# Kernel optimization log

Hardware: AMD Instinct MI355X
Metric: run time of the kernel (lower is better)

The kernel has to match this reference:

```python
import jax, jax.numpy as jnp
import numpy as np

N = 100000   # nodes
E = 1600000  # message edges (avg degree 16)
L = 500000   # supervision (label) edges
IN = 128     # input feature dim
H = 2        # attention heads
C = 64       # hidden_dim per head
HC = H * C   # 128, per-layer output channels
DEC = 64     # decoder_dim
NEG_SLOPE = 0.2


def setup_inputs():
    key = jax.random.key(0)
    ks = jax.random.split(key, 16)
    s = 0.05
    return {
        "x": jax.random.normal(ks[0], (N, IN), jnp.float32),
        "edge_index": jax.random.randint(ks[1], (2, E), 0, N, dtype=jnp.int64),
        "edge_label_index": jax.random.randint(ks[2], (2, L), 0, N, dtype=jnp.int64),
        "W1": jax.random.normal(ks[3], (IN, HC), jnp.float32) * s,
        "att_src1": jax.random.normal(ks[4], (H, C), jnp.float32) * s,
        "att_dst1": jax.random.normal(ks[5], (H, C), jnp.float32) * s,
        "bias1": jnp.zeros((HC,), jnp.float32),
        "W2": jax.random.normal(ks[6], (HC, HC), jnp.float32) * s,
        "att_src2": jax.random.normal(ks[7], (H, C), jnp.float32) * s,
        "att_dst2": jax.random.normal(ks[8], (H, C), jnp.float32) * s,
        "bias2": jnp.zeros((HC,), jnp.float32),
        "lin1_w": jax.random.normal(ks[9], (2 * HC, DEC), jnp.float32) * s,
        "lin1_b": jnp.zeros((DEC,), jnp.float32),
        "lin2_w": jax.random.normal(ks[10], (DEC, 1), jnp.float32) * s,
        "lin2_b": jnp.zeros((1,), jnp.float32),
    }


def _gat_conv(x, src, dst, W, att_src, att_dst, bias, n_nodes):
    # PyG GATConv (concat=True, negative_slope=0.2), self-loops already in src/dst.
    h = (x @ W).reshape(-1, H, C)                       # [N, H, C]
    a_s = jnp.sum(h * att_src[None], axis=-1)           # [N, H]
    a_d = jnp.sum(h * att_dst[None], axis=-1)           # [N, H]
    e = jax.nn.leaky_relu(a_s[src] + a_d[dst], NEG_SLOPE)  # [E, H]
    m = jax.ops.segment_max(e, dst, num_segments=n_nodes)  # segment-softmax (stable)
    ex = jnp.exp(e - jax.lax.stop_gradient(m)[dst])
    denom = jax.ops.segment_sum(ex, dst, num_segments=n_nodes)
    alpha = ex / denom[dst]                             # [E, H]
    out = jax.ops.segment_sum(h[src] * alpha[:, :, None], dst, num_segments=n_nodes)
    return out.reshape(n_nodes, HC) + bias


def reference(x, edge_index, edge_label_index, W1, att_src1, att_dst1, bias1,
              W2, att_src2, att_dst2, bias2, lin1_w, lin1_b, lin2_w, lin2_b):
    n = x.shape[0]
    loop = jnp.arange(n, dtype=edge_index.dtype)
    src = jnp.concatenate([edge_index[0], loop])
    dst = jnp.concatenate([edge_index[1], loop])
    # encode (eval mode: dropout is a no-op)
    h1 = jax.nn.relu(_gat_conv(x, src, dst, W1, att_src1, att_dst1, bias1, n))
    z = _gat_conv(h1, src, dst, W2, att_src2, att_dst2, bias2, n)
    # decode
    hs = jnp.concatenate([z[edge_label_index[0]], z[edge_label_index[1]]], axis=1)
    hdec = jax.nn.relu(hs @ lin1_w + lin1_b)
    return (hdec @ lin2_w + lin2_b).reshape(-1)
```

## Files before the change

### kernel.cpp

```cpp
#include <hip/hip_runtime.h>
#include <hip/hip_fp16.h>


typedef _Float16 f16x8 __attribute__((ext_vector_type(8)));
typedef float f32x4 __attribute__((ext_vector_type(4)));

__device__ __forceinline__ float rl_f(float v, int lane) {
    return __int_as_float(__builtin_amdgcn_readlane(__float_as_int(v), lane));
}

__device__ __forceinline__ void fma_mix_lo(float& acc, unsigned hv, float e) {
    asm("v_fma_mix_f32 %0, %1, %2, %0 op_sel_hi:[1,0,0]"
        : "+v"(acc) : "v"(hv), "v"(e));
}
__device__ __forceinline__ void fma_mix_hi(float& acc, unsigned hv, float e) {
    asm("v_fma_mix_f32 %0, %1, %2, %0 op_sel:[1,0,0] op_sel_hi:[1,0,0]"
        : "+v"(acc) : "v"(hv), "v"(e));
}

#define WT_LD 136
__global__ __launch_bounds__(256, 3) void gemm_mfma(
    const float* __restrict__ X, const float* __restrict__ W,
    _Float16* __restrict__ Y, int nrows,
    const float* __restrict__ att_s, const float* __restrict__ att_d,
    float2* __restrict__ as_out, float2* __restrict__ ad_out)
{
    __shared__ _Float16 WT[128 * WT_LD];
    __shared__ _Float16 At[64 * WT_LD];
    const int t = threadIdx.x;
    const int lane = t & 63;
    const int wid = t >> 6;

    for (int i = t; i < 128 * 32; i += 256) {
        const int k = i >> 5;
        const int n4 = (i & 31) * 4;
        const float4 wv = *reinterpret_cast<const float4*>(&W[k * 128 + n4]);
        WT[(n4 + 0) * WT_LD + k] = (_Float16)wv.x;
        WT[(n4 + 1) * WT_LD + k] = (_Float16)wv.y;
        WT[(n4 + 2) * WT_LD + k] = (_Float16)wv.z;
        WT[(n4 + 3) * WT_LD + k] = (_Float16)wv.w;
    }

    const int am = lane & 15, ag = lane >> 4;

    float asv[8], adv[8];
    if (as_out) {
#pragma unroll
        for (int n0 = 0; n0 < 8; ++n0) {
            asv[n0] = att_s[n0 * 16 + am];
            adv[n0] = att_d[n0 * 16 + am];
        }
    }

    const int ntiles = (nrows + 63) >> 6;
    for (int tile = blockIdx.x; tile < ntiles; tile += gridDim.x) {
        const int rbase = tile * 64;
        __syncthreads();
        {
            const int r = t >> 2;
            const int c0 = (t & 3) * 32;
            const int gr = rbase + r;
            _Float16 tmp[32];
            if (gr < nrows) {
                const float* src = X + (size_t)gr * 128 + c0;
#pragma unroll
                for (int q = 0; q < 8; ++q) {
                    const float4 v = *reinterpret_cast<const float4*>(src + q * 4);
                    tmp[q * 4 + 0] = (_Float16)v.x; tmp[q * 4 + 1] = (_Float16)v.y;
                    tmp[q * 4 + 2] = (_Float16)v.z; tmp[q * 4 + 3] = (_Float16)v.w;
                }
            } else {
#pragma unroll
                for (int q = 0; q < 32; ++q) tmp[q] = (_Float16)0.f;
            }
#pragma unroll
            for (int q = 0; q < 4; ++q)
                *reinterpret_cast<f16x8*>(&At[r * WT_LD + c0 + q * 8]) =
                    *reinterpret_cast<const f16x8*>(&tmp[q * 8]);
        }
        __syncthreads();

        const int srow = wid * 16;
        f16x8 a[4];
#pragma unroll
        for (int kb = 0; kb < 4; ++kb)
            a[kb] = *reinterpret_cast<const f16x8*>(
                &At[(srow + am) * WT_LD + kb * 32 + ag * 8]);

        f32x4 acc[8];
#pragma unroll
        for (int n0 = 0; n0 < 8; ++n0) {
            f32x4 c = {0.f, 0.f, 0.f, 0.f};
#pragma unroll
            for (int kb = 0; kb < 4; ++kb) {
                const f16x8 b = *reinterpret_cast<const f16x8*>(
                    &WT[(n0 * 16 + am) * WT_LD + kb * 32 + ag * 8]);
                c = __builtin_amdgcn_mfma_f32_16x16x32_f16(a[kb], b, c, 0, 0, 0);
            }
            acc[n0] = c;
        }

        const int growbase = rbase + srow + ag * 4;

#pragma unroll
        for (int j = 0; j < 4; ++j) {
            const int grow = growbase + j;
            if (grow < nrows) {
#pragma unroll
                for (int n0 = 0; n0 < 8; ++n0)
                    Y[(size_t)grow * 128 + n0 * 16 + am] = (_Float16)acc[n0][j];
            }
        }

        if (as_out) {
#pragma unroll
            for (int j = 0; j < 4; ++j) {
                float s0 = 0.f, s1 = 0.f, d0 = 0.f, d1 = 0.f;
#pragma unroll
                for (int n0 = 0; n0 < 4; ++n0) {
                    s0 = fmaf(acc[n0][j], asv[n0], s0);
                    d0 = fmaf(acc[n0][j], adv[n0], d0);
                }
#pragma unroll
                for (int n0 = 4; n0 < 8; ++n0) {
                    s1 = fmaf(acc[n0][j], asv[n0], s1);
                    d1 = fmaf(acc[n0][j], adv[n0], d1);
                }
#pragma unroll
                for (int off = 1; off < 16; off <<= 1) {
                    s0 += __shfl_xor(s0, off, 64); s1 += __shfl_xor(s1, off, 64);
                    d0 += __shfl_xor(d0, off, 64); d1 += __shfl_xor(d1, off, 64);
                }
                const int grow = growbase + j;
                if (am == 0 && grow < nrows) {
                    as_out[grow] = make_float2(s0, s1);
                    ad_out[grow] = make_float2(d0, d1);
                }
            }
        }
    }
}

__global__ __launch_bounds__(256) void init_counts_k(int* __restrict__ counts, int N)
{
    const int i = blockIdx.x * blockDim.x + threadIdx.x;
    if (i < N) counts[i] = 1;
}

__global__ __launch_bounds__(256) void hist_xcd_k(
    const int* __restrict__ edst, int E, int* __restrict__ counts, int npp)
{
    const int part = blockIdx.x & 7;
    const int lo = part * npp;
    const int hiN = lo + npp;
    const int bi = blockIdx.x >> 3;
    const int stride = (gridDim.x >> 3) * blockDim.x;
    for (int e = bi * blockDim.x + threadIdx.x; e < E; e += stride) {
        const int d = edst[e];
        if (d >= lo && d < hiN) atomicAdd(&counts[d], 1);
    }
}

__global__ __launch_bounds__(256) void scan_phase1(
    const int* __restrict__ counts, int* __restrict__ blockSums, int N)
{
    __shared__ int wsum[4];
    const int b = blockIdx.x, t = threadIdx.x;
    const int base = b * 1024 + t * 4;
    int s = 0;
    if (base + 3 < N) {
        const int4 c = *reinterpret_cast<const int4*>(&counts[base]);
        s = c.x + c.y + c.z + c.w;
    } else {
#pragma unroll
        for (int k = 0; k < 4; ++k) if (base + k < N) s += counts[base + k];
    }
#pragma unroll
    for (int off = 32; off; off >>= 1) s += __shfl_xor(s, off, 64);
    if ((t & 63) == 0) wsum[t >> 6] = s;
    __syncthreads();
    if (t == 0) blockSums[b] = wsum[0] + wsum[1] + wsum[2] + wsum[3];
}

__global__ __launch_bounds__(256) void scan_phase2(
    int* __restrict__ blockSums, int nb, int* __restrict__ row_ptr, int N)
{
    __shared__ int wsum[4];
    __shared__ int carry_sh;
    const int t = threadIdx.x;
    if (t == 0) carry_sh = 0;
    __syncthreads();
    for (int base = 0; base < nb; base += 256) {
        const int i = base + t;
        const int v = (i < nb) ? blockSums[i] : 0;
        int x = v;
#pragma unroll
        for (int off = 1; off < 64; off <<= 1) {
            const int y = __shfl_up(x, off, 64);
            if ((t & 63) >= off) x += y;
        }
        if ((t & 63) == 63) wsum[t >> 6] = x;
        __syncthreads();
        int woff = 0;
        for (int w = 0; w < (t >> 6); ++w) woff += wsum[w];
        const int carry = carry_sh;
        if (i < nb) blockSums[i] = carry + woff + x - v;
        __syncthreads();
        if (t == 255) carry_sh = carry + woff + x;
        __syncthreads();
    }
    if (t == 0) row_ptr[N] = carry_sh;
}

__global__ __launch_bounds__(256) void scan_phase3(
    const int* __restrict__ counts, const int* __restrict__ blockSums,
    int* __restrict__ row_ptr, int N)
{
    __shared__ int wsum[4];
    const int b = blockIdx.x, t = threadIdx.x;
    const int base = b * 1024 + t * 4;
    int v0 = 0, v1 = 0, v2 = 0, v3 = 0;
    if (base + 3 < N) {
        const int4 c = *reinterpret_cast<const int4*>(&counts[base]);
        v0 = c.x; v1 = c.y; v2 = c.z; v3 = c.w;
    } else {
        if (base + 0 < N) v0 = counts[base + 0];
        if (base + 1 < N) v1 = counts[base + 1];
        if (base + 2 < N) v2 = counts[base + 2];
        if (base + 3 < N) v3 = counts[base + 3];
    }
    const int tsum = v0 + v1 + v2 + v3;
    int x = tsum;
#pragma unroll
    for (int off = 1; off < 64; off <<= 1) {
        const int y = __shfl_up(x, off, 64);
        if ((t & 63) >= off) x += y;
    }
    if ((t & 63) == 63) wsum[t >> 6] = x;
    __syncthreads();
    int woff = 0;
    for (int w = 0; w < (t >> 6); ++w) woff += wsum[w];
    int excl = blockSums[b] + woff + x - tsum;
    if (base + 0 < N) row_ptr[base + 0] = excl;
    if (base + 1 < N) row_ptr[base + 1] = excl + v0;
    if (base + 2 < N) row_ptr[base + 2] = excl + v0 + v1;
    if (base + 3 < N) row_ptr[base + 3] = excl + v0 + v1 + v2;
}

__global__ __launch_bounds__(256) void init_cursor_k(
    const int* __restrict__ row_ptr, int* __restrict__ cursor,
    int* __restrict__ csr_src, int N)
{
    const int i = blockIdx.x * blockDim.x + threadIdx.x;
    if (i < N) {
        const int p = row_ptr[i];
        csr_src[p] = i;
        cursor[i] = p + 1;
    }
}

__global__ __launch_bounds__(256) void scatter_xcd_k(
    const int* __restrict__ esrc, const int* __restrict__ edst, int E,
    int* __restrict__ cursor, int* __restrict__ csr_src, int npp)
{
    const int part = blockIdx.x & 7;
    const int lo = part * npp;
    const int hiN = lo + npp;
    const int bi = blockIdx.x >> 3;
    const int stride = (gridDim.x >> 3) * blockDim.x;
    for (int e = bi * blockDim.x + threadIdx.x; e < E; e += stride) {
        const int d = edst[e];
        if (d >= lo && d < hiN) {
            const int pos = atomicAdd(&cursor[d], 1);
            csr_src[pos] = esrc[e];
        }
    }
}

__global__ __launch_bounds__(256) void csr_aggregate(
    const int* __restrict__ row_ptr, const int* __restrict__ csr_src,
    const unsigned* __restrict__ h2u, const float2* __restrict__ as_,
    const float2* __restrict__ ad_, const float* __restrict__ bias,
    float* __restrict__ out, int N, int do_relu)
{
    const int lane = threadIdx.x & 63;
    const int node = (blockIdx.x * blockDim.x + threadIdx.x) >> 6;
    if (node >= N) return;
    const int l32 = lane & 31;
    const int half = lane >> 5;
    const bool head1 = l32 >= 16;

    const int start = row_ptr[node];
    const int end   = row_ptr[node + 1];
    const float2 ad = ad_[node];

    float den0 = 0.f, den1 = 0.f;
    float acc0 = 0.f, acc1 = 0.f, acc2 = 0.f, acc3 = 0.f;

    for (int base = start; base < end; base += 64) {
        const int cnt = min(64, end - base);
        float ex0 = 0.f, ex1 = 0.f;
        int s = 0;
        if (lane < cnt) {
            s = csr_src[base + lane];
            const float2 as = as_[s];
            float e0 = as.x + ad.x; e0 = fmaxf(e0, 0.2f * e0);
            float e1 = as.y + ad.y; e1 = fmaxf(e1, 0.2f * e1);
            ex0 = __expf(e0); ex1 = __expf(e1);
            den0 += ex0; den1 += ex1;
        }
        int j = 0;
        for (; j + 8 <= cnt; j += 8) {
            uint2 hv[4]; float e[4];
#pragma unroll
            for (int q = 0; q < 4; ++q) {
                const int jA = j + 2 * q, jB = jA + 1;
                const int sA = __builtin_amdgcn_readlane(s, jA);
                const int sB = __builtin_amdgcn_readlane(s, jB);
                const float eA = head1 ? rl_f(ex1, jA) : rl_f(ex0, jA);
                const float eB = head1 ? rl_f(ex1, jB) : rl_f(ex0, jB);
                e[q] = half ? eB : eA;
                const int src = half ? sB : sA;
                hv[q] = *reinterpret_cast<const uint2*>(
                    h2u + (unsigned)(src * 64 + l32 * 2));
            }
#pragma unroll
            for (int q = 0; q < 4; ++q) {
                fma_mix_lo(acc0, hv[q].x, e[q]);
                fma_mix_hi(acc1, hv[q].x, e[q]);
                fma_mix_lo(acc2, hv[q].y, e[q]);
                fma_mix_hi(acc3, hv[q].y, e[q]);
            }
        }
        for (; j < cnt; j += 2) {
            const int jA = j, jB = j + 1;
            const int sA = __builtin_amdgcn_readlane(s, jA);
            const int sB = __builtin_amdgcn_readlane(s, jB);
            const float eA = head1 ? rl_f(ex1, jA) : rl_f(ex0, jA);
            const float eB = head1 ? rl_f(ex1, jB) : rl_f(ex0, jB);
            const float e = half ? eB : eA;
            const int src = half ? sB : sA;
            const uint2 hv = *reinterpret_cast<const uint2*>(
                h2u + (unsigned)(src * 64 + l32 * 2));
            fma_mix_lo(acc0, hv.x, e);
            fma_mix_hi(acc1, hv.x, e);
            fma_mix_lo(acc2, hv.y, e);
            fma_mix_hi(acc3, hv.y, e);
        }
    }

    acc0 += __shfl_xor(acc0, 32, 64);
    acc1 += __shfl_xor(acc1, 32, 64);
    acc2 += __shfl_xor(acc2, 32, 64);
    acc3 += __shfl_xor(acc3, 32, 64);

#pragma unroll
    for (int off = 32; off; off >>= 1) {
        den0 += __shfl_xor(den0, off, 64);
        den1 += __shfl_xor(den1, off, 64);
    }

    if (half == 0) {
        const float rd = 1.f / (head1 ? den1 : den0);
        const float4 bv = *reinterpret_cast<const float4*>(&bias[l32 * 4]);
        float4 v;
        v.x = fmaf(acc0, rd, bv.x);
        v.y = fmaf(acc1, rd, bv.y);
        v.z = fmaf(acc2, rd, bv.z);
        v.w = fmaf(acc3, rd, bv.w);
        if (do_relu) {
            v.x = fmaxf(v.x, 0.f); v.y = fmaxf(v.y, 0.f);
            v.z = fmaxf(v.z, 0.f); v.w = fmaxf(v.w, 0.f);
        }
        *reinterpret_cast<float4*>(&out[(size_t)node * 128 + l32 * 4]) = v;
    }
}

__global__ void build_wuv(const float* __restrict__ lin1_w, float* __restrict__ Wuv)
{
    const int i = blockIdx.x * blockDim.x + threadIdx.x;
    if (i >= 128 * 128) return;
    const int k = i >> 7, j = i & 127;
    Wuv[i] = (j < 64) ? lin1_w[k * 64 + j] : lin1_w[(128 + k) * 64 + (j - 64)];
}

__global__ __launch_bounds__(256) void decode_k(
    const int* __restrict__ eli, int L_, const unsigned* __restrict__ uvd,
    const float* __restrict__ lin1_b, const float* __restrict__ lin2_w,
    const float* __restrict__ lin2_b, float* __restrict__ out)
{
    const int lane = threadIdx.x & 63;
    const int l32 = lane & 31;
    const int half = lane >> 5;
    const int pstride = (gridDim.x * blockDim.x) >> 6;
    const float2 bv = ((const float2*)lin1_b)[l32];
    const float2 wv = ((const float2*)lin2_w)[l32];
    const float b2 = lin2_b[0];
    const int npairs = (L_ + 1) >> 1;
    for (int pid = (blockIdx.x * blockDim.x + threadIdx.x) >> 6; pid < npairs; pid += pstride) {
        const int w = min(pid * 2 + half, L_ - 1);
        const int a = eli[w], b = eli[L_ + w];
        const unsigned ua = uvd[(unsigned)(a * 64 + l32)];
        const unsigned vb = uvd[(unsigned)(b * 64 + 32 + l32)];
        float x0 = bv.x, x1 = bv.y;
        asm("v_fma_mix_f32 %0, %1, 1.0, %0 op_sel_hi:[1,0,0]" : "+v"(x0) : "v"(ua));
        asm("v_fma_mix_f32 %0, %1, 1.0, %0 op_sel:[1,0,0] op_sel_hi:[1,0,0]" : "+v"(x1) : "v"(ua));
        asm("v_fma_mix_f32 %0, %1, 1.0, %0 op_sel_hi:[1,0,0]" : "+v"(x0) : "v"(vb));
        asm("v_fma_mix_f32 %0, %1, 1.0, %0 op_sel:[1,0,0] op_sel_hi:[1,0,0]" : "+v"(x1) : "v"(vb));
        x0 = fmaxf(x0, 0.f); x1 = fmaxf(x1, 0.f);
        float p = fmaf(x0, wv.x, x1 * wv.y);
#pragma unroll
        for (int off = 1; off < 32; off <<= 1) p += __shfl_xor(p, off, 64);
        if (l32 == 0 && pid * 2 + half < L_) out[pid * 2 + half] = p + b2;
    }
}

extern "C" void kernel_launch(void* const* d_in, const int* in_sizes, int n_in,
                              void* d_out, int out_size, void* d_ws, size_t ws_size,
                              hipStream_t stream)
{
    const float* x     = (const float*)d_in[0];
    const int*   ei    = (const int*)d_in[1];
    const int*   eli   = (const int*)d_in[2];
    const float* W1    = (const float*)d_in[3];
    const float* atts1 = (const float*)d_in[4];
    const float* attd1 = (const float*)d_in[5];
    const float* bias1 = (const float*)d_in[6];
    const float* W2    = (const float*)d_in[7];
    const float* atts2 = (const float*)d_in[8];
    const float* attd2 = (const float*)d_in[9];
    const float* bias2 = (const float*)d_in[10];
    const float* lin1w = (const float*)d_in[11];
    const float* lin1b = (const float*)d_in[12];
    const float* lin2w = (const float*)d_in[13];
    const float* lin2b = (const float*)d_in[14];
    float* out = (float*)d_out;

    const int N = in_sizes[0] / 128;
    const int E = in_sizes[1] / 2;
    const int L = in_sizes[2] / 2;

    float* ws   = (float*)d_ws;
    __half2* h16 = (__half2*)ws;
    float* x2z  = ws + (size_t)N * 64;
    float* a_s  = x2z + (size_t)N * 128;
    float* a_d  = a_s + (size_t)N * 2;
    float* Wuv  = a_d + (size_t)N * 2;
    int* row_ptr = (int*)(Wuv + 128 * 128);
    int* counts  = row_ptr + (N + 4);
    int* cursor  = counts + N;
    int* csr_src = cursor + N;
    int* blockSums = csr_src + (E + N);

    const int nBlocks256 = (N + 255) / 256;
    const int nb = (N + 1023) / 1024;
    const int npp = (N + 7) / 8;
    const int ntiles = (N + 63) / 64;
    const int gemmGrid = ntiles < 768 ? ntiles : 768;

    init_counts_k<<<nBlocks256, 256, 0, stream>>>(counts, N);
    hist_xcd_k<<<2048, 256, 0, stream>>>(ei + E, E, counts, npp);
    scan_phase1<<<nb, 256, 0, stream>>>(counts, blockSums, N);
    scan_phase2<<<1, 256, 0, stream>>>(blockSums, nb, row_ptr, N);
    scan_phase3<<<nb, 256, 0, stream>>>(counts, blockSums, row_ptr, N);
    init_cursor_k<<<nBlocks256, 256, 0, stream>>>(row_ptr, cursor, csr_src, N);
    scatter_xcd_k<<<2048, 256, 0, stream>>>(ei, ei + E, E, cursor, csr_src, npp);

    for (int layer = 0; layer < 2; ++layer) {
        const float* xin  = (layer == 0) ? x : x2z;
        const float* W    = (layer == 0) ? W1 : W2;
        const float* as_w = (layer == 0) ? atts1 : atts2;
        const float* ad_w = (layer == 0) ? attd1 : attd2;
        const float* bs   = (layer == 0) ? bias1 : bias2;

        gemm_mfma<<<gemmGrid, 256, 0, stream>>>(xin, W, (_Float16*)h16, N, as_w, ad_w,
                                                (float2*)a_s, (float2*)a_d);
        csr_aggregate<<<(N + 3) / 4, 256, 0, stream>>>(row_ptr, csr_src,
                                                       (const unsigned*)h16,
                                                       (const float2*)a_s, (const float2*)a_d,
                                                       bs, x2z, N, (layer == 0) ? 1 : 0);
    }

    build_wuv<<<64, 256, 0, stream>>>(lin1w, Wuv);
    gemm_mfma<<<gemmGrid, 256, 0, stream>>>(x2z, Wuv, (_Float16*)h16, N,
                                            nullptr, nullptr, nullptr, nullptr);
    decode_k<<<8192, 256, 0, stream>>>(eli, L, (const unsigned*)h16,
                                       lin1b, lin2w, lin2b, out);
}
```

Baseline: 438.0 us.

## Prefetch next GEMM tile into registers and fuse CSR init into scan

The GEMM kernel now loads the next 64-row tile of X into registers while the MFMA work on the current tile runs, hiding global-load latency in the persistent loop at the cost of extra registers. CSR construction drops the counts-init and cursor-init kernels. Counts are zeroed with a memset, the self-loop +1 is added inside the scan phases, and scan_phase3 writes row_ptr, the self-loop csr_src entry and the cursor directly. This removes two kernel launches and one pass over row_ptr.

Measured after the change: 431.0 us. About the same (-1.6%).

```diff
diff --git a/kernel.cpp b/kernel.cpp
--- a/kernel.cpp
+++ b/kernel.cpp
@@ -42,6 +42,8 @@
     }
 
     const int am = lane & 15, ag = lane >> 4;
+    const int pr = t >> 2;
+    const int pc = (t & 3) * 32;
 
     float asv[8], adv[8];
     if (as_out) {
@@ -52,33 +54,44 @@
         }
     }
 
+    float4 pf[8];
+    auto load_pf = [&](int tbase) {
+        const int gr = tbase + pr;
+        if (gr < nrows) {
+            const float* src = X + (size_t)gr * 128 + pc;
+#pragma unroll
+            for (int q = 0; q < 8; ++q)
+                pf[q] = *reinterpret_cast<const float4*>(src + q * 4);
+        } else {
+#pragma unroll
+            for (int q = 0; q < 8; ++q) pf[q] = make_float4(0.f, 0.f, 0.f, 0.f);
+        }
+    };
+    auto write_pf = [&]() {
+        _Float16 tmp[32];
+#pragma unroll
+        for (int q = 0; q < 8; ++q) {
+            tmp[q * 4 + 0] = (_Float16)pf[q].x; tmp[q * 4 + 1] = (_Float16)pf[q].y;
+            tmp[q * 4 + 2] = (_Float16)pf[q].z; tmp[q * 4 + 3] = (_Float16)pf[q].w;
+        }
+#pragma unroll
+        for (int q = 0; q < 4; ++q)
+            *reinterpret_cast<f16x8*>(&At[pr * WT_LD + pc + q * 8]) =
+                *reinterpret_cast<const f16x8*>(&tmp[q * 8]);
+    };
+
     const int ntiles = (nrows + 63) >> 6;
-    for (int tile = blockIdx.x; tile < ntiles; tile += gridDim.x) {
+    int tile = blockIdx.x;
+    if (tile < ntiles) load_pf(tile * 64);
+
+    for (; tile < ntiles; tile += gridDim.x) {
         const int rbase = tile * 64;
         __syncthreads();
-        {
-            const int r = t >> 2;
-            const int c0 = (t & 3) * 32;
-            const int gr = rbase + r;
-            _Float16 tmp[32];
-            if (gr < nrows) {
-                const float* src = X + (size_t)gr * 128 + c0;
-#pragma unroll
-                for (int q = 0; q < 8; ++q) {
-                    const float4 v = *reinterpret_cast<const float4*>(src + q * 4);
-                    tmp[q * 4 + 0] = (_Float16)v.x; tmp[q * 4 + 1] = (_Float16)v.y;
-                    tmp[q * 4 + 2] = (_Float16)v.z; tmp[q * 4 + 3] = (_Float16)v.w;
-                }
-            } else {
-#pragma unroll
-                for (int q = 0; q < 32; ++q) tmp[q] = (_Float16)0.f;
-            }
-#pragma unroll
-            for (int q = 0; q < 4; ++q)
-                *reinterpret_cast<f16x8*>(&At[r * WT_LD + c0 + q * 8]) =
-                    *reinterpret_cast<const f16x8*>(&tmp[q * 8]);
-        }
+        write_pf();
         __syncthreads();
+
+        const int nt = tile + gridDim.x;
+        if (nt < ntiles) load_pf(nt * 64);
 
         const int srow = wid * 16;
         f16x8 a[4];
@@ -141,12 +154,6 @@
     }
 }
 
-__global__ __launch_bounds__(256) void init_counts_k(int* __restrict__ counts, int N)
-{
-    const int i = blockIdx.x * blockDim.x + threadIdx.x;
-    if (i < N) counts[i] = 1;
-}
-
 __global__ __launch_bounds__(256) void hist_xcd_k(
     const int* __restrict__ edst, int E, int* __restrict__ counts, int npp)
 {
@@ -170,10 +177,10 @@
     int s = 0;
     if (base + 3 < N) {
         const int4 c = *reinterpret_cast<const int4*>(&counts[base]);
-        s = c.x + c.y + c.z + c.w;
+        s = c.x + c.y + c.z + c.w + 4;
     } else {
 #pragma unroll
-        for (int k = 0; k < 4; ++k) if (base + k < N) s += counts[base + k];
+        for (int k = 0; k < 4; ++k) if (base + k < N) s += counts[base + k] + 1;
     }
 #pragma unroll
     for (int off = 32; off; off >>= 1) s += __shfl_xor(s, off, 64);
@@ -214,7 +221,8 @@
 
 __global__ __launch_bounds__(256) void scan_phase3(
     const int* __restrict__ counts, const int* __restrict__ blockSums,
-    int* __restrict__ row_ptr, int N)
+    int* __restrict__ row_ptr, int* __restrict__ cursor,
+    int* __restrict__ csr_src, int N)
 {
     __shared__ int wsum[4];
     const int b = blockIdx.x, t = threadIdx.x;
@@ -222,12 +230,12 @@
     int v0 = 0, v1 = 0, v2 = 0, v3 = 0;
     if (base + 3 < N) {
         const int4 c = *reinterpret_cast<const int4*>(&counts[base]);
-        v0 = c.x; v1 = c.y; v2 = c.z; v3 = c.w;
+        v0 = c.x + 1; v1 = c.y + 1; v2 = c.z + 1; v3 = c.w + 1;
     } else {
-        if (base + 0 < N) v0 = counts[base + 0];
-        if (base + 1 < N) v1 = counts[base + 1];
-        if (base + 2 < N) v2 = counts[base + 2];
-        if (base + 3 < N) v3 = counts[base + 3];
+        if (base + 0 < N) v0 = counts[base + 0] + 1;
+        if (base + 1 < N) v1 = counts[base + 1] + 1;
+        if (base + 2 < N) v2 = counts[base + 2] + 1;
+        if (base + 3 < N) v3 = counts[base + 3] + 1;
     }
     const int tsum = v0 + v1 + v2 + v3;
     int x = tsum;
@@ -241,22 +249,11 @@
     int woff = 0;
     for (int w = 0; w < (t >> 6); ++w) woff += wsum[w];
     int excl = blockSums[b] + woff + x - tsum;
-    if (base + 0 < N) row_ptr[base + 0] = excl;
-    if (base + 1 < N) row_ptr[base + 1] = excl + v0;
-    if (base + 2 < N) row_ptr[base + 2] = excl + v0 + v1;
-    if (base + 3 < N) row_ptr[base + 3] = excl + v0 + v1 + v2;
-}
-
-__global__ __launch_bounds__(256) void init_cursor_k(
-    const int* __restrict__ row_ptr, int* __restrict__ cursor,
-    int* __restrict__ csr_src, int N)
-{
-    const int i = blockIdx.x * blockDim.x + threadIdx.x;
-    if (i < N) {
-        const int p = row_ptr[i];
-        csr_src[p] = i;
-        cursor[i] = p + 1;
-    }
+    int p = excl;
+    if (base + 0 < N) { row_ptr[base + 0] = p; csr_src[p] = base + 0; cursor[base + 0] = p + 1; p += v0; }
+    if (base + 1 < N) { row_ptr[base + 1] = p; csr_src[p] = base + 1; cursor[base + 1] = p + 1; p += v1; }
+    if (base + 2 < N) { row_ptr[base + 2] = p; csr_src[p] = base + 2; cursor[base + 2] = p + 1; p += v2; }
+    if (base + 3 < N) { row_ptr[base + 3] = p; csr_src[p] = base + 3; cursor[base + 3] = p + 1; }
 }
 
 __global__ __launch_bounds__(256) void scatter_xcd_k(
@@ -452,18 +449,16 @@
     int* csr_src = cursor + N;
     int* blockSums = csr_src + (E + N);
 
-    const int nBlocks256 = (N + 255) / 256;
     const int nb = (N + 1023) / 1024;
     const int npp = (N + 7) / 8;
     const int ntiles = (N + 63) / 64;
     const int gemmGrid = ntiles < 768 ? ntiles : 768;
 
-    init_counts_k<<<nBlocks256, 256, 0, stream>>>(counts, N);
+    hipMemsetAsync(counts, 0, (size_t)N * sizeof(int), stream);
     hist_xcd_k<<<2048, 256, 0, stream>>>(ei + E, E, counts, npp);
     scan_phase1<<<nb, 256, 0, stream>>>(counts, blockSums, N);
     scan_phase2<<<1, 256, 0, stream>>>(blockSums, nb, row_ptr, N);
-    scan_phase3<<<nb, 256, 0, stream>>>(counts, blockSums, row_ptr, N);
-    init_cursor_k<<<nBlocks256, 256, 0, stream>>>(row_ptr, cursor, csr_src, N);
+    scan_phase3<<<nb, 256, 0, stream>>>(counts, blockSums, row_ptr, cursor, csr_src, N);
     scatter_xcd_k<<<2048, 256, 0, stream>>>(ei, ei + E, E, cursor, csr_src, npp);
 
     for (int layer = 0; layer < 2; ++layer) {
```
